# Performance work log

Measured on AMD Instinct MI355X. Metric: run time of the kernel, lower is better.

Reference implementation:

```python
import jax, jax.numpy as jnp
import numpy as np
import math

EMBED_DIM = 128
NUM_HEADS = 8
HEAD_DIM = EMBED_DIM // NUM_HEADS
# Faithful to the source's concat bug: heads [0,1,1,2,3,4,5,6] (head 7 dropped, head 1 duplicated)
HEAD_ORDER = [0, 1, 1, 2, 3, 4, 5, 6]


def setup_inputs() -> dict:
    key = jax.random.key(0)
    ks = jax.random.split(key, 7)
    B, S = 4, 2048
    input_embeddings = jax.random.normal(ks[0], (B, S, EMBED_DIM), dtype=jnp.float32)
    token_attention_masks = jax.random.randint(ks[1], (B, S), 0, 2, dtype=jnp.int64)
    # torch.rand -> uniform [0,1)
    w_query = jax.random.uniform(ks[2], (EMBED_DIM, EMBED_DIM), dtype=jnp.float32)
    w_key = jax.random.uniform(ks[3], (EMBED_DIM, EMBED_DIM), dtype=jnp.float32)
    w_value = jax.random.uniform(ks[4], (EMBED_DIM, EMBED_DIM), dtype=jnp.float32)
    # nn.Linear params
    lim = 1.0 / math.sqrt(EMBED_DIM)
    lin_w = jax.random.uniform(ks[5], (EMBED_DIM, EMBED_DIM), dtype=jnp.float32, minval=-lim, maxval=lim)
    lin_b = jax.random.uniform(ks[6], (EMBED_DIM,), dtype=jnp.float32, minval=-lim, maxval=lim)
    return {"input_embeddings": input_embeddings, "token_attention_masks": token_attention_masks,
            "w_query": w_query, "w_key": w_key, "w_value": w_value, "lin_w": lin_w, "lin_b": lin_b}


def reference(input_embeddings, token_attention_masks, w_query, w_key, w_value, lin_w, lin_b):
    B, S, _ = input_embeddings.shape
    q = input_embeddings @ w_query  # [B,S,D]
    k = input_embeddings @ w_key
    v = input_embeddings @ w_value
    # split heads: [B,S,H,hd] -> [B,H,S,hd]
    qh = q.reshape(B, S, NUM_HEADS, HEAD_DIM).transpose(0, 2, 1, 3)
    kh = k.reshape(B, S, NUM_HEADS, HEAD_DIM).transpose(0, 2, 1, 3)
    vh = v.reshape(B, S, NUM_HEADS, HEAD_DIM).transpose(0, 2, 1, 3)
    # NOTE: source scales by sqrt(full embedding dim), not sqrt(head_dim)
    scale = 1.0 / math.sqrt(EMBED_DIM)
    scores = jnp.einsum('bhsd,bhtd->bhst', qh, kh) * scale  # [B,H,S,S]
    # mask: 0 -> -1000, 1 -> 0; broadcast over query positions
    mask = jnp.where(token_attention_masks == 0, -1000.0, 0.0).astype(scores.dtype)  # [B,S]
    scores = scores + mask[:, None, None, :]
    probs = jax.nn.softmax(scores, axis=-1)
    out_h = jnp.einsum('bhst,bhtd->bhsd', probs, vh)  # [B,H,S,hd]
    # buggy concat order kept faithful
    attn_out = jnp.concatenate([out_h[:, i] for i in HEAD_ORDER], axis=-1)  # [B,S,D]
    return attn_out @ lin_w.T + lin_b
```

## Files before the change

kernel.cpp:

```cpp
#include <hip/hip_runtime.h>
#include <stdint.h>

typedef unsigned short u16;
typedef unsigned int   u32;
typedef int     i32x4  __attribute__((ext_vector_type(4)));
typedef float   f32x4  __attribute__((ext_vector_type(4)));
typedef float   f32x16 __attribute__((ext_vector_type(16)));
typedef __bf16  bf16x8 __attribute__((ext_vector_type(8)));
typedef u32     u32x4  __attribute__((ext_vector_type(4)));
typedef u32     u32x2  __attribute__((ext_vector_type(2)));

union BF8 { bf16x8 v; u16 s[8]; u32x4 q; };

__device__ __forceinline__ u16 f2b_rne(float f) {
    u32 u = __builtin_bit_cast(u32, f);
    u32 r = u + 0x7FFFu + ((u >> 16) & 1u);
    return (u16)(r >> 16);
}
__device__ __forceinline__ u16 f2b_trunc(float f) {
    return (u16)(__builtin_bit_cast(u32, f) >> 16);
}
__device__ __forceinline__ float b2f(u16 h) {
    u32 u = ((u32)h) << 16;
    return __builtin_bit_cast(float, u);
}
__device__ __forceinline__ bf16x8 ld_bf8(const u16* p) {
    BF8 t; t.q = *(const u32x4*)p; return t.v;
}
__device__ __forceinline__ f32x16 zero16() {
    f32x16 z;
#pragma unroll
    for (int i = 0; i < 16; i++) z[i] = 0.f;
    return z;
}
__device__ __forceinline__ f32x4 zero4() {
    f32x4 z;
#pragma unroll
    for (int i = 0; i < 4; i++) z[i] = 0.f;
    return z;
}

#define SCALE2 0.1275312959479341f

__device__ __forceinline__ void st_ao(u16* aob, int row, int col, u16 v) {
    int blk = (col >> 3) ^ (row & 15);
    aob[row * 128 + blk * 8 + (col & 7)] = v;
}

__global__ __launch_bounds__(256) void proj_kernel(
    const float* __restrict__ x, const float* __restrict__ wq,
    const float* __restrict__ wk, const float* __restrict__ wv,
    const int* __restrict__ mask, int* __restrict__ Larr,
    u16* Qph, u16* Qpl, u16* Kph, u16* Kpl, u16* VT)
{
    int typ  = blockIdx.y;
    int ct   = threadIdx.x >> 6;
    int lane = threadIdx.x & 63;
    int m = lane & 31, kg = lane >> 5;
    int r0 = blockIdx.x * 32;
    int c = ct * 32 + m;
    int b = r0 >> 11, sl = r0 & 2047;

    __shared__ int pos_sh[32];
    __shared__ int Lsh;

    if (typ != 0) {
        if (threadIdx.x < 64) {
            int tl = threadIdx.x;
            const int* mp = mask + b * 2048 + tl * 32;
            int mv[32]; int cntv = 0;
#pragma unroll
            for (int j4 = 0; j4 < 8; j4++) {
                i32x4 t = *(const i32x4*)(mp + j4 * 4);
#pragma unroll
                for (int q = 0; q < 4; q++) {
                    mv[j4 * 4 + q] = t[q];
                    cntv += (t[q] != 0);
                }
            }
            int off = cntv;
#pragma unroll
            for (int d = 1; d < 64; d <<= 1) {
                int o = __shfl_up(off, d, 64);
                if (tl >= d) off += o;
            }
            if (tl == 63) Lsh = off;
            if (tl == (sl >> 5)) {
                int p = off - cntv;
#pragma unroll
                for (int j = 0; j < 32; j++) {
                    pos_sh[j] = mv[j] ? p : -1;
                    p += (mv[j] != 0);
                }
            }
        }
        __syncthreads();
    }

    const float* wp = (typ == 0) ? wq : (typ == 1) ? wk : wv;

    f32x16 acc = zero16();
#pragma unroll 4
    for (int kk = 0; kk < 128; kk += 16) {
        const float* xp = x + (size_t)(r0 + m) * 128 + kk + kg * 8;
        f32x4 x0 = *(const f32x4*)xp;
        f32x4 x1 = *(const f32x4*)(xp + 4);
        BF8 ah, al;
#pragma unroll
        for (int j = 0; j < 4; j++) {
            u16 hb = f2b_trunc(x0[j]);
            ah.s[j] = hb; al.s[j] = f2b_trunc(x0[j] - b2f(hb));
            u16 hb2 = f2b_trunc(x1[j]);
            ah.s[4 + j] = hb2; al.s[4 + j] = f2b_trunc(x1[j] - b2f(hb2));
        }
        const float* wcol = wp + (size_t)(kk + kg * 8) * 128 + c;
        if (typ < 2) {
            BF8 bh, bl_;
#pragma unroll
            for (int j = 0; j < 8; j++) {
                float w = wcol[(size_t)j * 128];
                u16 hb = f2b_trunc(w);
                bh.s[j] = hb; bl_.s[j] = f2b_trunc(w - b2f(hb));
            }
            acc = __builtin_amdgcn_mfma_f32_32x32x16_bf16(ah.v, bh.v, acc, 0, 0, 0);
            acc = __builtin_amdgcn_mfma_f32_32x32x16_bf16(ah.v, bl_.v, acc, 0, 0, 0);
            acc = __builtin_amdgcn_mfma_f32_32x32x16_bf16(al.v, bh.v, acc, 0, 0, 0);
        } else {
            BF8 bh;
#pragma unroll
            for (int j = 0; j < 8; j++) bh.s[j] = f2b_rne(wcol[(size_t)j * 128]);
            acc = __builtin_amdgcn_mfma_f32_32x32x16_bf16(ah.v, bh.v, acc, 0, 0, 0);
        }
    }

    int hh = c >> 4, d = c & 15;
    if (typ == 0) {
        if (hh == 7) return;
        size_t hb_off = (size_t)(b * 8 + hh) * 2048 * 16 + d;
#pragma unroll
        for (int r = 0; r < 16; r++) {
            int row = (r & 3) + 8 * (r >> 2) + 4 * kg;
            float v = acc[r] * SCALE2;
            u16 hi = f2b_trunc(v);
            size_t idx = hb_off + (size_t)(sl + row) * 16;
            Qph[idx] = hi;
            Qpl[idx] = f2b_trunc(v - b2f(hi));
        }
    } else if (typ == 1) {
        if (hh == 7) return;
        size_t hb_off = (size_t)(b * 8 + hh) * 2048 * 16 + d;
#pragma unroll
        for (int r = 0; r < 16; r++) {
            int row = (r & 3) + 8 * (r >> 2) + 4 * kg;
            int p = pos_sh[row];
            if (p < 0) continue;
            float v = acc[r];
            u16 hi = f2b_trunc(v);
            size_t idx = hb_off + (size_t)p * 16;
            Kph[idx] = hi;
            Kpl[idx] = f2b_trunc(v - b2f(hi));
        }
    } else {
        if (hh != 7) {
#pragma unroll
            for (int rg = 0; rg < 4; rg++) {
#pragma unroll
                for (int q = 0; q < 4; q++) {
                    int row = rg * 8 + 4 * kg + q;
                    int p = pos_sh[row];
                    if (p >= 0)
                        VT[(size_t)(b * 128 + c) * 2048 + p] = f2b_rne(acc[rg * 4 + q]);
                }
            }
        }
        int L = Lsh;
        int npad = (L + 127) & ~127; if (npad < 128) npad = 128;
        int padn = npad - L;
        int slice = blockIdx.x & 63;
        if (padn > 0) {
            int e = slice * 256 + threadIdx.x;
            int k = e & 127, cc = e >> 7;
            if (k < padn) VT[(size_t)(b * 128 + cc) * 2048 + (L + k)] = 0;
        }
        if (slice == 0 && threadIdx.x == 0) Larr[b] = L;
    }
}

__global__ __launch_bounds__(448, 2) void attn_kernel(
    const u16* __restrict__ Qph, const u16* __restrict__ Qpl,
    const u16* __restrict__ Kph, const u16* __restrict__ Kpl,
    const u16* __restrict__ VT, const int* __restrict__ Larr,
    const float* __restrict__ lw, const float* __restrict__ lb,
    float* __restrict__ out)
{
    __shared__ char smem[22528];
    u16* pbuf = (u16*)smem;
    u16* aob  = (u16*)(smem + 14336);

    int bid = blockIdx.x;
    int b = bid >> 6, qt = bid & 63;
    int wave = threadIdx.x >> 6;
    int lane = threadIdx.x & 63;
    int m = lane & 31, kg = lane >> 5;
    int qs = qt * 32;
    int h = wave;

    int L = Larr[b];
    int npad = (L + 127) & ~127; if (npad < 128) npad = 128;

    size_t headoff = (size_t)(b * 8 + h) * 2048 * 16;
    bf16x8 qfh = ld_bf8(Qph + headoff + (size_t)(qs + m) * 16 + kg * 8);
    bf16x8 qfl = ld_bf8(Qpl + headoff + (size_t)(qs + m) * 16 + kg * 8);
    const u16* kbh = Kph + headoff;
    const u16* kbl = Kpl + headoff;

    float mloc = -3.0e38f;
    {
        bf16x8 khc = ld_bf8(kbh + (size_t)m * 16 + kg * 8);
        for (int t = 0; t < npad; t += 32) {
            int tn = (t + 32 < npad) ? (t + 32) : 0;
            bf16x8 khn = ld_bf8(kbh + (size_t)(tn + m) * 16 + kg * 8);
            f32x16 sc = __builtin_amdgcn_mfma_f32_32x32x16_bf16(khc, qfh, zero16(), 0, 0, 0);
            if (t + 32 <= L) {
#pragma unroll
                for (int r = 0; r < 16; r++) mloc = fmaxf(mloc, sc[r]);
            } else {
#pragma unroll
                for (int r = 0; r < 16; r++) {
                    int key = t + (r & 3) + 8 * (r >> 2) + 4 * kg;
                    if (key < L) mloc = fmaxf(mloc, sc[r]);
                }
            }
            khc = khn;
        }
    }
    float mrow = fmaxf(mloc, __shfl_xor(mloc, 32, 64));

    f32x4 o0 = zero4(), o1 = zero4(), l0 = zero4(), l1 = zero4();
    BF8 onesu;
#pragma unroll
    for (int j = 0; j < 8; j++) onesu.s[j] = 0x3F80;
    bf16x8 ones = onesu.v;

    int q16 = lane & 15, krow = lane >> 4;
    const u16* vtb = VT + (size_t)(b * 128 + h * 16 + q16) * 2048;
    int msw = (m >> 1) & 3;
    int qsw = (q16 >> 1) & 3;
    u16* pwb = pbuf + wave * 1024 + m * 32 + kg * 4;
    const u16* pr0 = pbuf + wave * 1024 + q16 * 32 + ((krow ^ qsw) * 8);
    const u16* pr1 = pr0 + 16 * 32;

    bf16x8 khc = ld_bf8(kbh + (size_t)m * 16 + kg * 8);
    bf16x8 klc = ld_bf8(kbl + (size_t)m * 16 + kg * 8);

    for (int t = 0; t < npad; t += 32) {
        int tn = (t + 32 < npad) ? (t + 32) : 0;
        bf16x8 khn = ld_bf8(kbh + (size_t)(tn + m) * 16 + kg * 8);
        bf16x8 kln = ld_bf8(kbl + (size_t)(tn + m) * 16 + kg * 8);
        bf16x8 vf  = ld_bf8(vtb + t + krow * 8);

        f32x16 sc = zero16();
        sc = __builtin_amdgcn_mfma_f32_32x32x16_bf16(khc, qfl, sc, 0, 0, 0);
        sc = __builtin_amdgcn_mfma_f32_32x32x16_bf16(klc, qfh, sc, 0, 0, 0);
        sc = __builtin_amdgcn_mfma_f32_32x32x16_bf16(khc, qfh, sc, 0, 0, 0);
        bool tail = (t + 32 > L);
#pragma unroll
        for (int rg = 0; rg < 4; rg++) {
            float e0 = __builtin_amdgcn_exp2f(sc[rg * 4 + 0] - mrow);
            float e1 = __builtin_amdgcn_exp2f(sc[rg * 4 + 1] - mrow);
            float e2 = __builtin_amdgcn_exp2f(sc[rg * 4 + 2] - mrow);
            float e3 = __builtin_amdgcn_exp2f(sc[rg * 4 + 3] - mrow);
            if (tail) {
                int kb = t + rg * 8 + kg * 4;
                e0 = (kb + 0 < L) ? e0 : 0.f;
                e1 = (kb + 1 < L) ? e1 : 0.f;
                e2 = (kb + 2 < L) ? e2 : 0.f;
                e3 = (kb + 3 < L) ? e3 : 0.f;
            }
            u32x2 pk;
            pk[0] = __builtin_amdgcn_perm(__builtin_bit_cast(u32, e1),
                                          __builtin_bit_cast(u32, e0), 0x07060302u);
            pk[1] = __builtin_amdgcn_perm(__builtin_bit_cast(u32, e3),
                                          __builtin_bit_cast(u32, e2), 0x07060302u);
            *(u32x2*)(pwb + ((rg ^ msw) * 8)) = pk;
        }
        bf16x8 p0 = *(const bf16x8*)pr0;
        bf16x8 p1 = *(const bf16x8*)pr1;
        o0 = __builtin_amdgcn_mfma_f32_16x16x32_bf16(p0, vf, o0, 0, 0, 0);
        o1 = __builtin_amdgcn_mfma_f32_16x16x32_bf16(p1, vf, o1, 0, 0, 0);
        l0 = __builtin_amdgcn_mfma_f32_16x16x32_bf16(p0, ones, l0, 0, 0, 0);
        l1 = __builtin_amdgcn_mfma_f32_16x16x32_bf16(p1, ones, l1, 0, 0, 0);
        khc = khn; klc = kln;
    }

    int slot0 = (h == 0) ? 0 : h + 1;
#pragma unroll
    for (int j = 0; j < 4; j++) {
        int row0 = krow * 4 + j;
        u16 v0 = f2b_rne(o0[j] * __builtin_amdgcn_rcpf(l0[j]));
        u16 v1 = f2b_rne(o1[j] * __builtin_amdgcn_rcpf(l1[j]));
        int col = slot0 * 16 + q16;
        st_ao(aob, row0,      col, v0);
        st_ao(aob, row0 + 16, col, v1);
        if (h == 1) {
            st_ao(aob, row0,      16 + q16, v0);
            st_ao(aob, row0 + 16, 16 + q16, v1);
        }
    }

    __syncthreads();
    if (threadIdx.x >= 256) return;

    int ct2 = threadIdx.x >> 6;
    int c = ct2 * 32 + m;
    int r0 = b * 2048 + qs;
    f32x16 acc = zero16();
#pragma unroll 4
    for (int kk = 0; kk < 128; kk += 16) {
        int col0 = kk + kg * 8;
        int blk = (col0 >> 3) ^ (m & 15);
        bf16x8 af = *(const bf16x8*)(aob + m * 128 + blk * 8);
        const float* wp2 = lw + (size_t)c * 128 + col0;
        f32x4 w0 = *(const f32x4*)wp2;
        f32x4 w1 = *(const f32x4*)(wp2 + 4);
        BF8 bfr;
#pragma unroll
        for (int j = 0; j < 4; j++) {
            bfr.s[j]     = f2b_rne(w0[j]);
            bfr.s[4 + j] = f2b_rne(w1[j]);
        }
        acc = __builtin_amdgcn_mfma_f32_32x32x16_bf16(af, bfr.v, acc, 0, 0, 0);
    }
    float bias = lb[c];
#pragma unroll
    for (int r = 0; r < 16; r++) {
        int row = (r & 3) + 8 * (r >> 2) + 4 * kg;
        out[(size_t)(r0 + row) * 128 + c] = acc[r] + bias;
    }
}

extern "C" void kernel_launch(void* const* d_in, const int* in_sizes, int n_in,
                              void* d_out, int out_size, void* d_ws, size_t ws_size,
                              hipStream_t stream)
{
    const float* x    = (const float*)d_in[0];
    const int*   mask = (const int*)d_in[1];
    const float* wq   = (const float*)d_in[2];
    const float* wk   = (const float*)d_in[3];
    const float* wv   = (const float*)d_in[4];
    const float* lw   = (const float*)d_in[5];
    const float* lb   = (const float*)d_in[6];
    float* out = (float*)d_out;

    char* ws = (char*)d_ws;
    u16* Qph = (u16*)(ws + 0 * 2097152);
    u16* Qpl = (u16*)(ws + 1 * 2097152);
    u16* Kph = (u16*)(ws + 2 * 2097152);
    u16* Kpl = (u16*)(ws + 3 * 2097152);
    u16* VT  = (u16*)(ws + 4 * 2097152);
    int* Larr = (int*)(ws + 5 * 2097152);

    proj_kernel<<<dim3(256, 3), 256, 0, stream>>>(x, wq, wk, wv, mask, Larr,
                                                  Qph, Qpl, Kph, Kpl, VT);
    attn_kernel<<<256, 448, 0, stream>>>(Qph, Qpl, Kph, Kpl, VT, Larr,
                                         lw, lb, out);
}
```

Before: 110.6 us.

## Fuse projection and attention kernels into one cooperative launch with grid sync

Merges the projection kernel and the attention kernel into a single cooperative kernel of 256 blocks of 448 threads. Each wave takes projection work items in a grid-stride loop, then a grid-wide barrier separates the projection phase from attention. The aim is to remove the second launch and the gap between the two kernels. In exchange, projection now runs with a different occupancy and work split, the mask prefix scan is repeated per wave, and cooperative grid sync has its own cost.

```diff
diff --git a/kernel.cpp b/kernel.cpp
--- a/kernel.cpp
+++ b/kernel.cpp
@@ -1,5 +1,8 @@
 #include <hip/hip_runtime.h>
+#include <hip/hip_cooperative_groups.h>
 #include <stdint.h>
+
+namespace cg = cooperative_groups;
 
 typedef unsigned short u16;
 typedef unsigned int   u32;
@@ -47,161 +50,160 @@
     aob[row * 128 + blk * 8 + (col & 7)] = v;
 }
 
-__global__ __launch_bounds__(256) void proj_kernel(
+__global__ __launch_bounds__(448, 2) void fused_kernel(
     const float* __restrict__ x, const float* __restrict__ wq,
     const float* __restrict__ wk, const float* __restrict__ wv,
-    const int* __restrict__ mask, int* __restrict__ Larr,
-    u16* Qph, u16* Qpl, u16* Kph, u16* Kpl, u16* VT)
-{
-    int typ  = blockIdx.y;
-    int ct   = threadIdx.x >> 6;
-    int lane = threadIdx.x & 63;
-    int m = lane & 31, kg = lane >> 5;
-    int r0 = blockIdx.x * 32;
-    int c = ct * 32 + m;
-    int b = r0 >> 11, sl = r0 & 2047;
-
-    __shared__ int pos_sh[32];
-    __shared__ int Lsh;
-
-    if (typ != 0) {
-        if (threadIdx.x < 64) {
-            int tl = threadIdx.x;
-            const int* mp = mask + b * 2048 + tl * 32;
-            int mv[32]; int cntv = 0;
-#pragma unroll
-            for (int j4 = 0; j4 < 8; j4++) {
-                i32x4 t = *(const i32x4*)(mp + j4 * 4);
-#pragma unroll
-                for (int q = 0; q < 4; q++) {
-                    mv[j4 * 4 + q] = t[q];
-                    cntv += (t[q] != 0);
-                }
-            }
-            int off = cntv;
-#pragma unroll
-            for (int d = 1; d < 64; d <<= 1) {
-                int o = __shfl_up(off, d, 64);
-                if (tl >= d) off += o;
-            }
-            if (tl == 63) Lsh = off;
-            if (tl == (sl >> 5)) {
-                int p = off - cntv;
-#pragma unroll
-                for (int j = 0; j < 32; j++) {
-                    pos_sh[j] = mv[j] ? p : -1;
-                    p += (mv[j] != 0);
-                }
-            }
-        }
-        __syncthreads();
-    }
-
-    const float* wp = (typ == 0) ? wq : (typ == 1) ? wk : wv;
-
-    f32x16 acc = zero16();
-#pragma unroll 4
-    for (int kk = 0; kk < 128; kk += 16) {
-        const float* xp = x + (size_t)(r0 + m) * 128 + kk + kg * 8;
-        f32x4 x0 = *(const f32x4*)xp;
-        f32x4 x1 = *(const f32x4*)(xp + 4);
-        BF8 ah, al;
-#pragma unroll
-        for (int j = 0; j < 4; j++) {
-            u16 hb = f2b_trunc(x0[j]);
-            ah.s[j] = hb; al.s[j] = f2b_trunc(x0[j] - b2f(hb));
-            u16 hb2 = f2b_trunc(x1[j]);
-            ah.s[4 + j] = hb2; al.s[4 + j] = f2b_trunc(x1[j] - b2f(hb2));
-        }
-        const float* wcol = wp + (size_t)(kk + kg * 8) * 128 + c;
-        if (typ < 2) {
-            BF8 bh, bl_;
-#pragma unroll
-            for (int j = 0; j < 8; j++) {
-                float w = wcol[(size_t)j * 128];
-                u16 hb = f2b_trunc(w);
-                bh.s[j] = hb; bl_.s[j] = f2b_trunc(w - b2f(hb));
-            }
-            acc = __builtin_amdgcn_mfma_f32_32x32x16_bf16(ah.v, bh.v, acc, 0, 0, 0);
-            acc = __builtin_amdgcn_mfma_f32_32x32x16_bf16(ah.v, bl_.v, acc, 0, 0, 0);
-            acc = __builtin_amdgcn_mfma_f32_32x32x16_bf16(al.v, bh.v, acc, 0, 0, 0);
-        } else {
-            BF8 bh;
-#pragma unroll
-            for (int j = 0; j < 8; j++) bh.s[j] = f2b_rne(wcol[(size_t)j * 128]);
-            acc = __builtin_amdgcn_mfma_f32_32x32x16_bf16(ah.v, bh.v, acc, 0, 0, 0);
-        }
-    }
-
-    int hh = c >> 4, d = c & 15;
-    if (typ == 0) {
-        if (hh == 7) return;
-        size_t hb_off = (size_t)(b * 8 + hh) * 2048 * 16 + d;
-#pragma unroll
-        for (int r = 0; r < 16; r++) {
-            int row = (r & 3) + 8 * (r >> 2) + 4 * kg;
-            float v = acc[r] * SCALE2;
-            u16 hi = f2b_trunc(v);
-            size_t idx = hb_off + (size_t)(sl + row) * 16;
-            Qph[idx] = hi;
-            Qpl[idx] = f2b_trunc(v - b2f(hi));
-        }
-    } else if (typ == 1) {
-        if (hh == 7) return;
-        size_t hb_off = (size_t)(b * 8 + hh) * 2048 * 16 + d;
-#pragma unroll
-        for (int r = 0; r < 16; r++) {
-            int row = (r & 3) + 8 * (r >> 2) + 4 * kg;
-            int p = pos_sh[row];
-            if (p < 0) continue;
-            float v = acc[r];
-            u16 hi = f2b_trunc(v);
-            size_t idx = hb_off + (size_t)p * 16;
-            Kph[idx] = hi;
-            Kpl[idx] = f2b_trunc(v - b2f(hi));
-        }
-    } else {
-        if (hh != 7) {
-#pragma unroll
-            for (int rg = 0; rg < 4; rg++) {
-#pragma unroll
-                for (int q = 0; q < 4; q++) {
-                    int row = rg * 8 + 4 * kg + q;
-                    int p = pos_sh[row];
-                    if (p >= 0)
-                        VT[(size_t)(b * 128 + c) * 2048 + p] = f2b_rne(acc[rg * 4 + q]);
-                }
-            }
-        }
-        int L = Lsh;
-        int npad = (L + 127) & ~127; if (npad < 128) npad = 128;
-        int padn = npad - L;
-        int slice = blockIdx.x & 63;
-        if (padn > 0) {
-            int e = slice * 256 + threadIdx.x;
-            int k = e & 127, cc = e >> 7;
-            if (k < padn) VT[(size_t)(b * 128 + cc) * 2048 + (L + k)] = 0;
-        }
-        if (slice == 0 && threadIdx.x == 0) Larr[b] = L;
-    }
-}
-
-__global__ __launch_bounds__(448, 2) void attn_kernel(
-    const u16* __restrict__ Qph, const u16* __restrict__ Qpl,
-    const u16* __restrict__ Kph, const u16* __restrict__ Kpl,
-    const u16* __restrict__ VT, const int* __restrict__ Larr,
+    const int* __restrict__ mask,
     const float* __restrict__ lw, const float* __restrict__ lb,
-    float* __restrict__ out)
+    u16* Qph, u16* Qpl, u16* Kph, u16* Kpl, u16* VT,
+    int* Larr, float* __restrict__ out)
 {
     __shared__ char smem[22528];
-    u16* pbuf = (u16*)smem;
-    u16* aob  = (u16*)(smem + 14336);
-
-    int bid = blockIdx.x;
-    int b = bid >> 6, qt = bid & 63;
     int wave = threadIdx.x >> 6;
     int lane = threadIdx.x & 63;
     int m = lane & 31, kg = lane >> 5;
+
+    {
+        int* wbuf = (int*)smem + wave * 32;
+        int gw = blockIdx.x * 7 + wave;
+
+        for (int item = gw; item < 3072; item += 1792) {
+            int typ = item >> 10;
+            int sub = item & 1023;
+            int xb = sub >> 2, ct = sub & 3;
+            int r0 = xb * 32;
+            int b = r0 >> 11, sl = r0 & 2047;
+            int c = ct * 32 + m;
+            int Lw = 0;
+
+            if (typ != 0) {
+                const int* mp = mask + b * 2048 + lane * 32;
+                int mv[32]; int cntv = 0;
+#pragma unroll
+                for (int j4 = 0; j4 < 8; j4++) {
+                    i32x4 t = *(const i32x4*)(mp + j4 * 4);
+#pragma unroll
+                    for (int q = 0; q < 4; q++) {
+                        mv[j4 * 4 + q] = t[q];
+                        cntv += (t[q] != 0);
+                    }
+                }
+                int off = cntv;
+#pragma unroll
+                for (int d = 1; d < 64; d <<= 1) {
+                    int o = __shfl_up(off, d, 64);
+                    if (lane >= d) off += o;
+                }
+                Lw = __shfl(off, 63, 64);
+                int src = xb & 63;
+                if (lane == src) {
+                    int p = off - cntv;
+#pragma unroll
+                    for (int j = 0; j < 32; j++) {
+                        wbuf[j] = mv[j] ? p : -1;
+                        p += (mv[j] != 0);
+                    }
+                }
+            }
+
+            const float* wp = (typ == 0) ? wq : (typ == 1) ? wk : wv;
+            f32x16 acc = zero16();
+#pragma unroll 4
+            for (int kk = 0; kk < 128; kk += 16) {
+                const float* xp = x + (size_t)(r0 + m) * 128 + kk + kg * 8;
+                f32x4 x0 = *(const f32x4*)xp;
+                f32x4 x1 = *(const f32x4*)(xp + 4);
+                BF8 ah, al;
+#pragma unroll
+                for (int j = 0; j < 4; j++) {
+                    u16 hb = f2b_trunc(x0[j]);
+                    ah.s[j] = hb; al.s[j] = f2b_trunc(x0[j] - b2f(hb));
+                    u16 hb2 = f2b_trunc(x1[j]);
+                    ah.s[4 + j] = hb2; al.s[4 + j] = f2b_trunc(x1[j] - b2f(hb2));
+                }
+                const float* wcol = wp + (size_t)(kk + kg * 8) * 128 + c;
+                if (typ < 2) {
+                    BF8 bh, bl_;
+#pragma unroll
+                    for (int j = 0; j < 8; j++) {
+                        float w = wcol[(size_t)j * 128];
+                        u16 hb = f2b_trunc(w);
+                        bh.s[j] = hb; bl_.s[j] = f2b_trunc(w - b2f(hb));
+                    }
+                    acc = __builtin_amdgcn_mfma_f32_32x32x16_bf16(ah.v, bh.v, acc, 0, 0, 0);
+                    acc = __builtin_amdgcn_mfma_f32_32x32x16_bf16(ah.v, bl_.v, acc, 0, 0, 0);
+                    acc = __builtin_amdgcn_mfma_f32_32x32x16_bf16(al.v, bh.v, acc, 0, 0, 0);
+                } else {
+                    BF8 bh;
+#pragma unroll
+                    for (int j = 0; j < 8; j++) bh.s[j] = f2b_rne(wcol[(size_t)j * 128]);
+                    acc = __builtin_amdgcn_mfma_f32_32x32x16_bf16(ah.v, bh.v, acc, 0, 0, 0);
+                }
+            }
+
+            int hh = c >> 4, d = c & 15;
+            if (typ == 0) {
+                if (hh != 7) {
+                    size_t hb_off = (size_t)(b * 8 + hh) * 2048 * 16 + d;
+#pragma unroll
+                    for (int r = 0; r < 16; r++) {
+                        int row = (r & 3) + 8 * (r >> 2) + 4 * kg;
+                        float v = acc[r] * SCALE2;
+                        u16 hi = f2b_trunc(v);
+                        size_t idx = hb_off + (size_t)(sl + row) * 16;
+                        Qph[idx] = hi;
+                        Qpl[idx] = f2b_trunc(v - b2f(hi));
+                    }
+                }
+            } else if (typ == 1) {
+                if (hh != 7) {
+                    size_t hb_off = (size_t)(b * 8 + hh) * 2048 * 16 + d;
+#pragma unroll
+                    for (int r = 0; r < 16; r++) {
+                        int row = (r & 3) + 8 * (r >> 2) + 4 * kg;
+                        int p = wbuf[row];
+                        if (p < 0) continue;
+                        float v = acc[r];
+                        u16 hi = f2b_trunc(v);
+                        size_t idx = hb_off + (size_t)p * 16;
+                        Kph[idx] = hi;
+                        Kpl[idx] = f2b_trunc(v - b2f(hi));
+                    }
+                }
+            } else {
+                if (hh != 7) {
+#pragma unroll
+                    for (int rg = 0; rg < 4; rg++) {
+#pragma unroll
+                        for (int q = 0; q < 4; q++) {
+                            int row = rg * 8 + 4 * kg + q;
+                            int p = wbuf[row];
+                            if (p >= 0)
+                                VT[(size_t)(b * 128 + c) * 2048 + p] =
+                                    f2b_rne(acc[rg * 4 + q]);
+                        }
+                    }
+                }
+                int npad = (Lw + 127) & ~127; if (npad < 128) npad = 128;
+                int padn = npad - Lw;
+                int slice = xb & 63;
+                if (padn > 0) {
+                    int e = slice * 256 + ct * 64 + lane;
+                    int k = e & 127, cc = e >> 7;
+                    if (k < padn) VT[(size_t)(b * 128 + cc) * 2048 + (Lw + k)] = 0;
+                }
+                if (slice == 0 && ct == 0 && lane == 0) Larr[b] = Lw;
+            }
+        }
+    }
+
+    cg::this_grid().sync();
+
+    u16* pbuf = (u16*)smem;
+    u16* aob  = (u16*)(smem + 14336);
+
+    int bid = blockIdx.x;
+    int b = bid >> 6, qt = bid & 63;
     int qs = qt * 32;
     int h = wave;
 
@@ -360,8 +362,12 @@
     u16* VT  = (u16*)(ws + 4 * 2097152);
     int* Larr = (int*)(ws + 5 * 2097152);
 
-    proj_kernel<<<dim3(256, 3), 256, 0, stream>>>(x, wq, wk, wv, mask, Larr,
-                                                  Qph, Qpl, Kph, Kpl, VT);
-    attn_kernel<<<256, 448, 0, stream>>>(Qph, Qpl, Kph, Kpl, VT, Larr,
-                                         lw, lb, out);
-}
+    void* args[] = {
+        (void*)&x, (void*)&wq, (void*)&wk, (void*)&wv, (void*)&mask,
+        (void*)&lw, (void*)&lb,
+        (void*)&Qph, (void*)&Qpl, (void*)&Kph, (void*)&Kpl, (void*)&VT,
+        (void*)&Larr, (void*)&out
+    };
+    hipLaunchCooperativeKernel((void*)fused_kernel, dim3(256), dim3(448),
+                               args, 0, stream);
+}
```

Result: slower. 174.8 us (+58.1%).

## Replace two-pass softmax max with online lazy-rescaled running max

Applied to the files above, without the earlier changes.

Removes the separate first pass that computed the row maximum over all keys using hi-precision QK MFMAs. The max is now tracked online in the main loop. Rescaling of the output and sum accumulators happens only when a tile's max exceeds the running max by more than a threshold, and the scale factors are passed through a small LDS buffer to match the output MFMA layout. This saves a full sweep of K loads and MFMAs per block, at the cost of a per-tile max reduction, a shuffle, and an occasional rescale with an LDS round trip.

```diff
diff --git a/kernel.cpp b/kernel.cpp
--- a/kernel.cpp
+++ b/kernel.cpp
@@ -193,9 +193,10 @@
     const float* __restrict__ lw, const float* __restrict__ lb,
     float* __restrict__ out)
 {
-    __shared__ char smem[22528];
-    u16* pbuf = (u16*)smem;
-    u16* aob  = (u16*)(smem + 14336);
+    __shared__ char smem[23552];
+    u16*   pbuf = (u16*)smem;
+    u16*   aob  = (u16*)(smem + 14336);
+    float* sclb = (float*)(smem + 22528);
 
     int bid = blockIdx.x;
     int b = bid >> 6, qt = bid & 63;
@@ -214,29 +215,8 @@
     const u16* kbh = Kph + headoff;
     const u16* kbl = Kpl + headoff;
 
-    float mloc = -3.0e38f;
-    {
-        bf16x8 khc = ld_bf8(kbh + (size_t)m * 16 + kg * 8);
-        for (int t = 0; t < npad; t += 32) {
-            int tn = (t + 32 < npad) ? (t + 32) : 0;
-            bf16x8 khn = ld_bf8(kbh + (size_t)(tn + m) * 16 + kg * 8);
-            f32x16 sc = __builtin_amdgcn_mfma_f32_32x32x16_bf16(khc, qfh, zero16(), 0, 0, 0);
-            if (t + 32 <= L) {
-#pragma unroll
-                for (int r = 0; r < 16; r++) mloc = fmaxf(mloc, sc[r]);
-            } else {
-#pragma unroll
-                for (int r = 0; r < 16; r++) {
-                    int key = t + (r & 3) + 8 * (r >> 2) + 4 * kg;
-                    if (key < L) mloc = fmaxf(mloc, sc[r]);
-                }
-            }
-            khc = khn;
-        }
-    }
-    float mrow = fmaxf(mloc, __shfl_xor(mloc, 32, 64));
-
     f32x4 o0 = zero4(), o1 = zero4(), l0 = zero4(), l1 = zero4();
+    float m_run = -3.0e38f;
     BF8 onesu;
 #pragma unroll
     for (int j = 0; j < 8; j++) onesu.s[j] = 0x3F80;
@@ -249,6 +229,7 @@
     u16* pwb = pbuf + wave * 1024 + m * 32 + kg * 4;
     const u16* pr0 = pbuf + wave * 1024 + q16 * 32 + ((krow ^ qsw) * 8);
     const u16* pr1 = pr0 + 16 * 32;
+    float* scl = sclb + wave * 32;
 
     bf16x8 khc = ld_bf8(kbh + (size_t)m * 16 + kg * 8);
     bf16x8 klc = ld_bf8(kbl + (size_t)m * 16 + kg * 8);
@@ -264,12 +245,40 @@
         sc = __builtin_amdgcn_mfma_f32_32x32x16_bf16(klc, qfh, sc, 0, 0, 0);
         sc = __builtin_amdgcn_mfma_f32_32x32x16_bf16(khc, qfh, sc, 0, 0, 0);
         bool tail = (t + 32 > L);
+
+        float tmax = -3.0e38f;
+        if (!tail) {
+#pragma unroll
+            for (int r = 0; r < 16; r++) tmax = fmaxf(tmax, sc[r]);
+        } else {
+#pragma unroll
+            for (int r = 0; r < 16; r++) {
+                int key = t + (r & 3) + 8 * (r >> 2) + 4 * kg;
+                if (key < L) tmax = fmaxf(tmax, sc[r]);
+            }
+        }
+        tmax = fmaxf(tmax, __shfl_xor(tmax, 32, 64));
+
+        if (__any(tmax > m_run + 8.0f)) {
+            float mnew = fmaxf(m_run, tmax);
+            float s = __builtin_amdgcn_exp2f(m_run - mnew);
+            if (kg == 0) scl[m] = s;
+            m_run = mnew;
+            f32x4 s0 = *(const f32x4*)(scl + krow * 4);
+            f32x4 s1 = *(const f32x4*)(scl + krow * 4 + 16);
+#pragma unroll
+            for (int j = 0; j < 4; j++) {
+                o0[j] *= s0[j]; l0[j] *= s0[j];
+                o1[j] *= s1[j]; l1[j] *= s1[j];
+            }
+        }
+
 #pragma unroll
         for (int rg = 0; rg < 4; rg++) {
-            float e0 = __builtin_amdgcn_exp2f(sc[rg * 4 + 0] - mrow);
-            float e1 = __builtin_amdgcn_exp2f(sc[rg * 4 + 1] - mrow);
-            float e2 = __builtin_amdgcn_exp2f(sc[rg * 4 + 2] - mrow);
-            float e3 = __builtin_amdgcn_exp2f(sc[rg * 4 + 3] - mrow);
+            float e0 = __builtin_amdgcn_exp2f(sc[rg * 4 + 0] - m_run);
+            float e1 = __builtin_amdgcn_exp2f(sc[rg * 4 + 1] - m_run);
+            float e2 = __builtin_amdgcn_exp2f(sc[rg * 4 + 2] - m_run);
+            float e3 = __builtin_amdgcn_exp2f(sc[rg * 4 + 3] - m_run);
             if (tail) {
                 int kb = t + rg * 8 + kg * 4;
                 e0 = (kb + 0 < L) ? e0 : 0.f;
```

Measured after the change: 107.5 us, median of 2. 2.8% less time.
